# Performance work log

Hardware: AMD Instinct MI355X
Metric: run time of the kernel (lower is better)

Reference implementation:

```python
import jax, jax.numpy as jnp
import numpy as np


def _ffn(h, wu, wd):
    # SwiGLU: split w_up output into gate/up halves (torch chunk(2, dim=-1))
    gate, up = jnp.split(h @ wu, 2, axis=-1)
    return (jax.nn.silu(gate) * up) @ wd


def setup_inputs() -> dict:
    key = jax.random.key(0)
    ks = jax.random.split(key, 6)
    B, S, H, E, F = 4, 2048, 1024, 16, 512
    scale = 0.02
    x = jax.random.normal(ks[0], (B, S, H), dtype=jnp.float32)
    Wr = jax.random.normal(ks[1], (H, E), dtype=jnp.float32) * scale        # router (Linear, no bias)
    W_up = jax.random.normal(ks[2], (E, H, 2 * F), dtype=jnp.float32) * scale  # stacked expert w_up
    W_down = jax.random.normal(ks[3], (E, F, H), dtype=jnp.float32) * scale    # stacked expert w_down
    Ws_up = jax.random.normal(ks[4], (H, 2 * F), dtype=jnp.float32) * scale    # shared expert
    Ws_down = jax.random.normal(ks[5], (F, H), dtype=jnp.float32) * scale
    return {"x": x, "Wr": Wr, "W_up": W_up, "W_down": W_down,
            "Ws_up": Ws_up, "Ws_down": Ws_down, "num_active": 2}


def reference(x, Wr, W_up, W_down, Ws_up, Ws_down, num_active):
    B, S, H = x.shape
    E = Wr.shape[1]
    xf = x.reshape(-1, H)                     # [T, H]
    T = xf.shape[0]
    router_probs = jax.nn.softmax(xf @ Wr, axis=-1)            # [T, E]
    topk_p, topk_i = jax.lax.top_k(router_probs, num_active)   # [T, K]
    topk_p = topk_p / (topk_p.sum(-1, keepdims=True) + 1e-9)
    # dense per-token combine weights; 0 for non-selected experts, so the
    # dense per-expert compute below matches the masked gather/scatter math
    w = jnp.zeros((T, E), x.dtype).at[jnp.arange(T)[:, None], topk_i].set(topk_p)

    def step(acc, p):
        wu, wd, we = p                         # [H,2F], [F,H], [T]
        return acc + we[:, None] * _ffn(xf, wu, wd), None

    out, _ = jax.lax.scan(step, jnp.zeros_like(xf), (W_up, W_down, w.T))
    out = out + _ffn(xf, Ws_up, Ws_down)       # shared expert added to every token
    return out.reshape(B, S, H), router_probs
```

## Files before the change

kernel.cpp:

```cpp
#include <hip/hip_runtime.h>
#include <stdint.h>

#define T_TOK 8192
#define HD 1024
#define NE 16
#define NET 17
#define FD 512
#define CAP 8448
#define MAXWG 448
#define CPX 56

typedef unsigned int uint;
typedef unsigned short ushort;
typedef __attribute__((ext_vector_type(8))) __bf16 bf16x8;
typedef __attribute__((ext_vector_type(4))) float f32x4;

#define OFF_XBF   0ull
#define OFF_WUPT  16777216ull
#define OFF_WDT   52428800ull
#define OFF_ACT   70254592ull
#define OFF_EIDX  95420416ull
#define OFF_EW    95485952ull
#define OFF_TOK   95551488ull
#define OFF_WGT   96125952ull
#define OFF_META  96700416ull
#define OFF_SEL   96704512ull
#define WS_NEEDED (OFF_SEL + 131072ull)


__device__ __forceinline__ ushort f2bf(float f) {
    uint u = __float_as_uint(f);
    u += 0x7FFFu + ((u >> 16) & 1u);
    return (ushort)(u >> 16);
}
__device__ __forceinline__ float bf2f(ushort u) {
    return __uint_as_float(((uint)u) << 16);
}
__device__ __forceinline__ void gload16(const void* g, void* l) {
    __builtin_amdgcn_global_load_lds(
        (const __attribute__((address_space(1))) void*)g,
        (__attribute__((address_space(3))) void*)l, 16, 0, 0);
}

__global__ __launch_bounds__(1024) void k_router(const float* __restrict__ x,
                                                 const float* __restrict__ Wr,
                                                 float* __restrict__ probs,
                                                 ushort* __restrict__ xb,
                                                 int* __restrict__ tok,
                                                 float* __restrict__ wgt,
                                                 int4* __restrict__ sel) {
    __shared__ __align__(16) float wr_s[HD * NE];
    int tid = threadIdx.x;
    int t0 = blockIdx.x * 16;
#pragma unroll
    for (int i = 0; i < 4; ++i) {
        int idx = (i * 1024 + tid) * 4;
        *(float4*)(&wr_s[idx]) = *(const float4*)(Wr + idx);
    }
#pragma unroll
    for (int p = 0; p < 4; ++p) {
        int r = p * 4 + (tid >> 8);
        int c = (tid & 255) * 4;
        float4 v = *(const float4*)(x + (size_t)(t0 + r) * HD + c);
        ushort4 cc;
        cc.x = f2bf(v.x); cc.y = f2bf(v.y); cc.z = f2bf(v.z); cc.w = f2bf(v.w);
        *(ushort4*)(xb + (size_t)(t0 + r) * HD + c) = cc;
    }
    __syncthreads();
    int t = t0 + (tid >> 6);
    int sub = tid & 63;
    int e = sub & 15, kp = sub >> 4;
    const float* xg = x + (size_t)t * HD + kp * 256;
    const int wb = kp * 256 * NE + e;
    float s0 = 0.f, s1 = 0.f;
#pragma unroll 8
    for (int j = 0; j < 256; j += 4) {
        float4 v = *(const float4*)(xg + j);
        s0 = fmaf(v.x, wr_s[wb + (j + 0) * NE], s0);
        s1 = fmaf(v.y, wr_s[wb + (j + 1) * NE], s1);
        s0 = fmaf(v.z, wr_s[wb + (j + 2) * NE], s0);
        s1 = fmaf(v.w, wr_s[wb + (j + 3) * NE], s1);
    }
    float s = s0 + s1;
    s += __shfl_xor(s, 16);
    s += __shfl_xor(s, 32);
    float m = s;
#pragma unroll
    for (int w = 1; w < 16; w <<= 1) m = fmaxf(m, __shfl_xor(m, w));
    float p = __expf(s - m);
    float sum = p;
#pragma unroll
    for (int w = 1; w < 16; w <<= 1) sum += __shfl_xor(sum, w);
    p /= sum;
    if (kp == 0) probs[(size_t)t * NE + e] = p;
    float m1 = p;
#pragma unroll
    for (int w = 1; w < 16; w <<= 1) m1 = fmaxf(m1, __shfl_xor(m1, w));
    unsigned long long bal = __ballot(p == m1);
    int i1 = __ffs((int)((bal >> (kp * 16)) & 0xFFFFu)) - 1;
    float p2v = (e == i1) ? -1.f : p;
    float m2 = p2v;
#pragma unroll
    for (int w = 1; w < 16; w <<= 1) m2 = fmaxf(m2, __shfl_xor(m2, w));
    bal = __ballot(p2v == m2);
    int i2 = __ffs((int)((bal >> (kp * 16)) & 0xFFFFu)) - 1;
    if (sub == 0) {
        float inv2 = 1.f / (m1 + m2 + 1e-9f);
        sel[t] = make_int4(i1, i2, __float_as_int(m1 * inv2), __float_as_int(m2 * inv2));
        tok[16 * CAP + t] = t;
        wgt[16 * CAP + t] = 1.f;
    }
}

__global__ __launch_bounds__(1024) void k_bucket(const int4* __restrict__ sel,
                                                 int* __restrict__ tok,
                                                 float* __restrict__ wgt,
                                                 int2* __restrict__ inva,
                                                 int2* __restrict__ invb,
                                                 int* __restrict__ meta) {
    __shared__ int wcnt[16], wbase[16];
    int e = blockIdx.x;
    int wave = threadIdx.x >> 6;
    int lane = threadIdx.x & 63;
    unsigned long long ltmask = (1ull << lane) - 1ull;
    int tstart = wave * 512;
    int cnt = 0;
#pragma unroll
    for (int it = 0; it < 8; ++it) {
        int4 s = sel[tstart + it * 64 + lane];
        cnt += (int)__popcll(__ballot(s.x == e)) + (int)__popcll(__ballot(s.y == e));
    }
    if (lane == 0) wcnt[wave] = cnt;
    __syncthreads();
    if (threadIdx.x == 0) {
        int acc = 0;
#pragma unroll
        for (int w = 0; w < 16; ++w) { wbase[w] = acc; acc += wcnt[w]; }
        meta[e] = acc;
    }
    __syncthreads();
    int pos = wbase[wave];
#pragma unroll
    for (int it = 0; it < 8; ++it) {
        int t = tstart + it * 64 + lane;
        int4 s = sel[t];
        bool m1 = (s.x == e), m2 = (s.y == e);
        unsigned long long b1 = __ballot(m1), b2 = __ballot(m2);
        int c1 = (int)__popcll(b1);
        if (m1) {
            int q = pos + (int)__popcll(b1 & ltmask);
            tok[e * CAP + q] = t; wgt[e * CAP + q] = __int_as_float(s.z);
            inva[t] = make_int2(e, q);
        }
        if (m2) {
            int q = pos + c1 + (int)__popcll(b2 & ltmask);
            tok[e * CAP + q] = t; wgt[e * CAP + q] = __int_as_float(s.w);
            invb[t] = make_int2(e, q);
        }
        pos += c1 + (int)__popcll(b2);
    }
}

__global__ __launch_bounds__(256) void k_tup(const float* __restrict__ Wup,
                                             const float* __restrict__ Wsup,
                                             ushort* __restrict__ dst) {
    __shared__ __align__(16) float tile[64][68];
    int bid = blockIdx.x;
    int e = bid >> 8, rem = bid & 255;
    int h0 = (rem >> 4) * 64, n0 = (rem & 15) * 64;
    const float* src = (e < 16) ? (Wup + (size_t)e * HD * 1024) : Wsup;
    int tid = threadIdx.x;
    int rr = tid >> 4, cc = (tid & 15) * 4;
#pragma unroll
    for (int q = 0; q < 4; ++q) {
        float4 v = *(const float4*)(src + (size_t)(h0 + q * 16 + rr) * 1024 + n0 + cc);
        *(float4*)(&tile[q * 16 + rr][cc]) = v;
    }
    __syncthreads();
#pragma unroll
    for (int q = 0; q < 4; ++q) {
        int nl = q * 16 + rr;
        ushort4 o;
        o.x = f2bf(tile[cc + 0][nl]);
        o.y = f2bf(tile[cc + 1][nl]);
        o.z = f2bf(tile[cc + 2][nl]);
        o.w = f2bf(tile[cc + 3][nl]);
        *(ushort4*)(dst + (size_t)e * 1048576 + (size_t)(n0 + nl) * 1024 + h0 + cc) = o;
    }
}

__global__ __launch_bounds__(256) void k_tdn(const float* __restrict__ Wdn,
                                             const float* __restrict__ Wsdn,
                                             ushort* __restrict__ dst) {
    __shared__ __align__(16) float tile[64][68];
    int bid = blockIdx.x;
    int e = bid >> 7, rem = bid & 127;
    int f0 = (rem >> 4) * 64, h0 = (rem & 15) * 64;
    const float* src = (e < 16) ? (Wdn + (size_t)e * FD * HD) : Wsdn;
    int tid = threadIdx.x;
    int rr = tid >> 4, cc = (tid & 15) * 4;
#pragma unroll
    for (int q = 0; q < 4; ++q) {
        float4 v = *(const float4*)(src + (size_t)(f0 + q * 16 + rr) * 1024 + h0 + cc);
        *(float4*)(&tile[q * 16 + rr][cc]) = v;
    }
    __syncthreads();
#pragma unroll
    for (int q = 0; q < 4; ++q) {
        int hl = q * 16 + rr;
        ushort4 o;
        o.x = f2bf(tile[cc + 0][hl]);
        o.y = f2bf(tile[cc + 1][hl]);
        o.z = f2bf(tile[cc + 2][hl]);
        o.w = f2bf(tile[cc + 3][hl]);
        *(ushort4*)(dst + (size_t)e * 524288 + (size_t)(h0 + hl) * 512 + f0 + cc) = o;
    }
}

__global__ void k_finalize(int* __restrict__ meta, int* __restrict__ tok,
                           float* __restrict__ wgt) {
    __shared__ int sN[NET], sPad[NET];
    int tid = threadIdx.x;
    if (tid == 0) {
        meta[16] = T_TOK;
        int idx = 0, yoff = 0;
        for (int e = 0; e < NET; e++) {
            int n = meta[e];
            int padded = (n + 255) & ~255;
            sN[e] = n; sPad[e] = padded;
            meta[416 + e] = yoff;
            for (int i = 0; i < padded; i += 256) {
                meta[32 + idx] = e; meta[160 + idx] = i; meta[288 + idx] = yoff + i; idx++;
            }
            yoff += n;
        }
        meta[17] = idx;
    }
    __syncthreads();
    for (int e = 0; e < NET; e++)
        for (int i = sN[e] + tid; i < sPad[e]; i += 256) {
            tok[e * CAP + i] = 0; wgt[e * CAP + i] = 0.f;
        }
}

__global__ __launch_bounds__(512, 2) void k_up(const ushort* __restrict__ xb,
                                               const ushort* __restrict__ wupT,
                                               ushort* __restrict__ act,
                                               const int* __restrict__ tok,
                                               const int* __restrict__ meta) {
    __shared__ __align__(16) char smem[131072];
    int bid = blockIdx.x;
    int s = (bid & 7) * CPX + (bid >> 3);
    int rb = s >> 2, cb = s & 3;
    if (rb >= meta[17]) return;
    int e = meta[32 + rb], rloc = meta[160 + rb], abrow = meta[288 + rb];
    int ne = meta[e];
    int tid = threadIdx.x, lane = tid & 63, wave = tid >> 6;

    int srow = tid >> 3;
    int col16 = (tid & 7) << 4;
    int swz = col16 ^ ((srow & 7) << 4);
    const int listBase = e * CAP + rloc;
    int tokr[4];
#pragma unroll
    for (int i = 0; i < 4; i++) tokr[i] = tok[listBase + i * 64 + srow];
    const char* xbase = (const char*)xb;
    const char* wb = (const char*)wupT + (size_t)e * 2097152;
    int ldsl = wave * 1024;

    int wr = wave >> 1, wc = wave & 1;
    int lr = lane & 15, lk = lane >> 4;
    int aOff = (wr * 64 + lr) * 128;
    int bOff = (wc * 64 + lr) * 128;
    int kp0 = (lk * 16) ^ ((lr & 7) << 4);
    int kp1 = (64 + lk * 16) ^ ((lr & 7) << 4);

    f32x4 accg[4][4], accu[4][4];
#pragma unroll
    for (int m = 0; m < 4; m++)
#pragma unroll
        for (int n = 0; n < 4; n++) {
            accg[m][n] = (f32x4){0.f, 0.f, 0.f, 0.f};
            accu[m][n] = (f32x4){0.f, 0.f, 0.f, 0.f};
        }

#define STAGE_UP(KT, D)                                                                   \
    {                                                                                     \
        char* base = smem + (D) * 65536;                                                  \
        int kB = (KT) * 128;                                                              \
        _Pragma("unroll")                                                                 \
        for (int i = 0; i < 4; i++)                                                       \
            gload16(xbase + (size_t)tokr[i] * 2048 + kB + swz, base + i * 8192 + ldsl);   \
        _Pragma("unroll")                                                                 \
        for (int i = 0; i < 2; i++)                                                       \
            gload16(wb + (size_t)(cb * 128 + i * 64 + srow) * 2048 + kB + swz,            \
                    base + 32768 + i * 8192 + ldsl);                                      \
        _Pragma("unroll")                                                                 \
        for (int i = 0; i < 2; i++)                                                       \
            gload16(wb + (size_t)(512 + cb * 128 + i * 64 + srow) * 2048 + kB + swz,      \
                    base + 49152 + i * 8192 + ldsl);                                      \
    }

    STAGE_UP(0, 0);
    asm volatile("s_waitcnt vmcnt(0)" ::: "memory");
    __syncthreads();
    int cur = 0;
#pragma unroll 1
    for (int kt = 0; kt < 16; ++kt) {
        if (kt < 15) STAGE_UP(kt + 1, cur ^ 1);
        const char* A  = smem + cur * 65536;
        const char* Bg = A + 32768;
        const char* Bu = A + 49152;
#pragma unroll
        for (int kk = 0; kk < 2; kk++) {
            int kp = kk ? kp1 : kp0;
            bf16x8 a[4], bg[4], bu[4];
#pragma unroll
            for (int m = 0; m < 4; m++) a[m] = *(const bf16x8*)(A + aOff + m * 2048 + kp);
#pragma unroll
            for (int n = 0; n < 4; n++) bg[n] = *(const bf16x8*)(Bg + bOff + n * 2048 + kp);
#pragma unroll
            for (int n = 0; n < 4; n++) bu[n] = *(const bf16x8*)(Bu + bOff + n * 2048 + kp);
#pragma unroll
            for (int m = 0; m < 4; m++)
#pragma unroll
                for (int n = 0; n < 4; n++) {
                    accg[m][n] = __builtin_amdgcn_mfma_f32_16x16x32_bf16(a[m], bg[n], accg[m][n], 0, 0, 0);
                    accu[m][n] = __builtin_amdgcn_mfma_f32_16x16x32_bf16(a[m], bu[n], accu[m][n], 0, 0, 0);
                }
        }
        asm volatile("s_waitcnt vmcnt(0)" ::: "memory");
        __syncthreads();
        cur ^= 1;
    }
    ushort* actl = (ushort*)smem;
#pragma unroll
    for (int m = 0; m < 4; m++)
#pragma unroll
        for (int n = 0; n < 4; n++)
#pragma unroll
            for (int j = 0; j < 4; j++) {
                float gv = accg[m][n][j];
                float uv = accu[m][n][j];
                float av = (gv / (1.f + __expf(-gv))) * uv;
                int row = wr * 64 + m * 16 + lk * 4 + j;
                int col = wc * 64 + n * 16 + lr;
                actl[row * 128 + col] = f2bf(av);
            }
    __syncthreads();
#pragma unroll
    for (int p = 0; p < 8; p++) {
        int c = p * 512 + tid;
        int row = c >> 4, off = (c & 15) << 4;
        if (rloc + row < ne)
            *(uint4*)((char*)act + (size_t)(abrow + row) * 1024 + cb * 256 + off) =
                *(const uint4*)((const char*)actl + row * 256 + off);
    }
#undef STAGE_UP
}

__global__ __launch_bounds__(512, 2) void k_down(const ushort* __restrict__ act,
                                                 const ushort* __restrict__ wdT,
                                                 ushort* __restrict__ ybuf,
                                                 const float* __restrict__ wgt,
                                                 const int* __restrict__ meta) {
    __shared__ __align__(16) char smem[131072];
    int bid = blockIdx.x;
    int s = (bid & 7) * CPX + (bid >> 3);
    int rb = s >> 2, cb = s & 3;
    if (rb >= meta[17]) return;
    int e = meta[32 + rb], rloc = meta[160 + rb], abrow = meta[288 + rb];
    int ne = meta[e];
    int tid = threadIdx.x, lane = tid & 63, wave = tid >> 6;

    int srow = tid >> 3;
    int col16 = (tid & 7) << 4;
    int swz = col16 ^ ((srow & 7) << 4);
    const char* abase = (const char*)act + (size_t)abrow * 1024;
    const char* bbase = (const char*)wdT + (size_t)e * 1048576 + (size_t)cb * 256 * 1024;
    int ldsl = wave * 1024;

    int wr = wave >> 1, wc = wave & 1;
    int lr = lane & 15, lk = lane >> 4;
    int aOff = (wr * 64 + lr) * 128;
    int bOff = (wc * 128 + lr) * 128;
    int kp0 = (lk * 16) ^ ((lr & 7) << 4);
    int kp1 = (64 + lk * 16) ^ ((lr & 7) << 4);

    f32x4 acc[4][8];
#pragma unroll
    for (int m = 0; m < 4; m++)
#pragma unroll
        for (int n = 0; n < 8; n++) acc[m][n] = (f32x4){0.f, 0.f, 0.f, 0.f};

#define STAGE_DN(KT, D)                                                                  \
    {                                                                                    \
        char* base = smem + (D) * 65536;                                                 \
        int kB = (KT) * 128;                                                             \
        _Pragma("unroll")                                                                \
        for (int i = 0; i < 4; i++)                                                      \
            gload16(abase + (size_t)(i * 64 + srow) * 1024 + kB + swz,                   \
                    base + i * 8192 + ldsl);                                             \
        _Pragma("unroll")                                                                \
        for (int i = 0; i < 4; i++)                                                      \
            gload16(bbase + (size_t)(i * 64 + srow) * 1024 + kB + swz,                   \
                    base + 32768 + i * 8192 + ldsl);                                     \
    }

    STAGE_DN(0, 0);
    asm volatile("s_waitcnt vmcnt(0)" ::: "memory");
    __syncthreads();
    int cur = 0;
#pragma unroll 1
    for (int kt = 0; kt < 8; ++kt) {
        if (kt < 7) STAGE_DN(kt + 1, cur ^ 1);
        const char* A = smem + cur * 65536;
        const char* B = A + 32768;
#pragma unroll
        for (int kk = 0; kk < 2; kk++) {
            int kp = kk ? kp1 : kp0;
            bf16x8 a[4], b[8];
#pragma unroll
            for (int m = 0; m < 4; m++) a[m] = *(const bf16x8*)(A + aOff + m * 2048 + kp);
#pragma unroll
            for (int n = 0; n < 8; n++) b[n] = *(const bf16x8*)(B + bOff + n * 2048 + kp);
#pragma unroll
            for (int m = 0; m < 4; m++)
#pragma unroll
                for (int n = 0; n < 8; n++)
                    acc[m][n] = __builtin_amdgcn_mfma_f32_16x16x32_bf16(a[m], b[n], acc[m][n], 0, 0, 0);
        }
        asm volatile("s_waitcnt vmcnt(0)" ::: "memory");
        __syncthreads();
        cur ^= 1;
    }
    const int lb = e * CAP + rloc;
    ushort* yl = (ushort*)smem;
#pragma unroll
    for (int m = 0; m < 4; m++)
#pragma unroll
        for (int j = 0; j < 4; j++) {
            int row = wr * 64 + m * 16 + lk * 4 + j;
            float w = wgt[lb + row];
#pragma unroll
            for (int n = 0; n < 8; n++) {
                int col = wc * 128 + n * 16 + lr;
                yl[row * 256 + col] = f2bf(acc[m][n][j] * w);
            }
        }
    __syncthreads();
#pragma unroll
    for (int p = 0; p < 16; p++) {
        int c = p * 512 + tid;
        int row = c >> 5, off = (c & 31) << 4;
        if (rloc + row < ne)
            *(uint4*)((char*)ybuf + (size_t)(abrow + row) * 2048 + cb * 512 + off) =
                *(const uint4*)((const char*)yl + row * 512 + off);
    }
#undef STAGE_DN
}

__global__ __launch_bounds__(256) void k_combine(const ushort* __restrict__ y,
                                                 const int2* __restrict__ ia,
                                                 const int2* __restrict__ ib,
                                                 const int* __restrict__ meta,
                                                 float* __restrict__ out) {
    int t = blockIdx.x;
    int2 a = ia[t], b = ib[t];
    int r0 = (meta[416 + a.x] + a.y) << 10;
    int r1 = (meta[416 + b.x] + b.y) << 10;
    int rs = (meta[432] + t) << 10;
    int c = threadIdx.x << 2;
    ushort4 va = *(const ushort4*)(y + r0 + c);
    ushort4 vb = *(const ushort4*)(y + r1 + c);
    ushort4 vs = *(const ushort4*)(y + rs + c);
    float4 o;
    o.x = bf2f(va.x) + bf2f(vb.x) + bf2f(vs.x);
    o.y = bf2f(va.y) + bf2f(vb.y) + bf2f(vs.y);
    o.z = bf2f(va.z) + bf2f(vb.z) + bf2f(vs.z);
    o.w = bf2f(va.w) + bf2f(vb.w) + bf2f(vs.w);
    *(float4*)(out + ((size_t)t << 10) + c) = o;
}

extern "C" void kernel_launch(void* const* d_in, const int* in_sizes, int n_in,
                              void* d_out, int out_size, void* d_ws, size_t ws_size,
                              hipStream_t stream) {
    const float* x    = (const float*)d_in[0];
    const float* Wr   = (const float*)d_in[1];
    const float* Wup  = (const float*)d_in[2];
    const float* Wdn  = (const float*)d_in[3];
    const float* Wsup = (const float*)d_in[4];
    const float* Wsdn = (const float*)d_in[5];
    float* out = (float*)d_out;
    float* probs = out + (size_t)T_TOK * HD;

    if (ws_size < WS_NEEDED) return;

    char* ws = (char*)d_ws;
    ushort* xb    = (ushort*)(ws + OFF_XBF);
    ushort* wupT  = (ushort*)(ws + OFF_WUPT);
    ushort* wdT   = (ushort*)(ws + OFF_WDT);
    ushort* act   = (ushort*)(ws + OFF_ACT);
    int2*   inva  = (int2*)(ws + OFF_EIDX);
    int2*   invb  = (int2*)(ws + OFF_EW);
    int*    tok   = (int*)(ws + OFF_TOK);
    float*  wgt   = (float*)(ws + OFF_WGT);
    int*    meta  = (int*)(ws + OFF_META);
    int4*   sel   = (int4*)(ws + OFF_SEL);
    ushort* ybuf  = (ushort*)(ws + OFF_XBF);

    k_tup<<<NET * 256, 256, 0, stream>>>(Wup, Wsup, wupT);
    k_tdn<<<NET * 128, 256, 0, stream>>>(Wdn, Wsdn, wdT);
    k_router<<<T_TOK / 16, 1024, 0, stream>>>(x, Wr, probs, xb, tok, wgt, sel);
    k_bucket<<<NE, 1024, 0, stream>>>(sel, tok, wgt, inva, invb, meta);
    k_finalize<<<1, 256, 0, stream>>>(meta, tok, wgt);
    k_up<<<MAXWG, 512, 0, stream>>>(xb, wupT, act, tok, meta);
    k_down<<<MAXWG, 512, 0, stream>>>(act, wdT, ybuf, wgt, meta);
    k_combine<<<T_TOK, 256, 0, stream>>>(ybuf, inva, invb, meta, out);
}
```

Baseline: 184.9 us.

## Switch expert GEMMs to 4-stage 64-wide K pipeline with partial waitcnt

Both the up and down expert GEMM kernels move from a double-buffered 128-wide K tile, which waited on all loads every step, to a 4-slot ring of 64-wide K tiles. Loads run three stages ahead and use partial vmcnt waits, so global loads overlap MFMA work. The LDS layout drops the XOR swizzle for a plain 64-byte row stride, and MFMA sections are wrapped in s_setprio. The unswizzled layout may cause LDS bank conflicts on the fragment reads, and using only a raw s_barrier per step leaves less margin for reuse hazards in the ring.

```diff
diff --git a/kernel.cpp b/kernel.cpp
--- a/kernel.cpp
+++ b/kernel.cpp
@@ -257,23 +257,22 @@
     int ne = meta[e];
     int tid = threadIdx.x, lane = tid & 63, wave = tid >> 6;
 
-    int srow = tid >> 3;
-    int col16 = (tid & 7) << 4;
-    int swz = col16 ^ ((srow & 7) << 4);
+    int chunk = (tid & 3) << 4;
+    int tid16 = tid << 4;
     const int listBase = e * CAP + rloc;
-    int tokr[4];
-#pragma unroll
-    for (int i = 0; i < 4; i++) tokr[i] = tok[listBase + i * 64 + srow];
+    int r0 = tid >> 2;
+    int tokr0 = tok[listBase + r0];
+    int tokr1 = tok[listBase + 128 + r0];
     const char* xbase = (const char*)xb;
     const char* wb = (const char*)wupT + (size_t)e * 2097152;
-    int ldsl = wave * 1024;
+    const char* wbg = wb + (size_t)(cb * 128 + r0) * 2048;
+    const char* wbu = wb + (size_t)(512 + cb * 128 + r0) * 2048;
 
     int wr = wave >> 1, wc = wave & 1;
     int lr = lane & 15, lk = lane >> 4;
-    int aOff = (wr * 64 + lr) * 128;
-    int bOff = (wc * 64 + lr) * 128;
-    int kp0 = (lk * 16) ^ ((lr & 7) << 4);
-    int kp1 = (64 + lk * 16) ^ ((lr & 7) << 4);
+    int aoff  = (wr * 64 + lr) * 64 + lk * 16;
+    int bgoff = 16384 + (wc * 64 + lr) * 64 + lk * 16;
+    int buoff = 24576 + (wc * 64 + lr) * 64 + lk * 16;
 
     f32x4 accg[4][4], accu[4][4];
 #pragma unroll
@@ -284,55 +283,44 @@
             accu[m][n] = (f32x4){0.f, 0.f, 0.f, 0.f};
         }
 
-#define STAGE_UP(KT, D)                                                                   \
-    {                                                                                     \
-        char* base = smem + (D) * 65536;                                                  \
-        int kB = (KT) * 128;                                                              \
-        _Pragma("unroll")                                                                 \
-        for (int i = 0; i < 4; i++)                                                       \
-            gload16(xbase + (size_t)tokr[i] * 2048 + kB + swz, base + i * 8192 + ldsl);   \
-        _Pragma("unroll")                                                                 \
-        for (int i = 0; i < 2; i++)                                                       \
-            gload16(wb + (size_t)(cb * 128 + i * 64 + srow) * 2048 + kB + swz,            \
-                    base + 32768 + i * 8192 + ldsl);                                      \
-        _Pragma("unroll")                                                                 \
-        for (int i = 0; i < 2; i++)                                                       \
-            gload16(wb + (size_t)(512 + cb * 128 + i * 64 + srow) * 2048 + kB + swz,      \
-                    base + 49152 + i * 8192 + ldsl);                                      \
-    }
-
-    STAGE_UP(0, 0);
-    asm volatile("s_waitcnt vmcnt(0)" ::: "memory");
-    __syncthreads();
-    int cur = 0;
+#define STAGE_UP(KT)                                                          \
+    {                                                                         \
+        char* b_ = smem + ((KT) & 3) * 32768;                                 \
+        int kB_ = (KT) * 64;                                                  \
+        gload16(xbase + (size_t)tokr0 * 2048 + kB_ + chunk, b_ + tid16);      \
+        gload16(xbase + (size_t)tokr1 * 2048 + kB_ + chunk, b_ + 8192 + tid16); \
+        gload16(wbg + kB_ + chunk, b_ + 16384 + tid16);                       \
+        gload16(wbu + kB_ + chunk, b_ + 24576 + tid16);                       \
+    }
+
+    STAGE_UP(0); STAGE_UP(1); STAGE_UP(2);
 #pragma unroll 1
-    for (int kt = 0; kt < 16; ++kt) {
-        if (kt < 15) STAGE_UP(kt + 1, cur ^ 1);
-        const char* A  = smem + cur * 65536;
-        const char* Bg = A + 32768;
-        const char* Bu = A + 49152;
-#pragma unroll
-        for (int kk = 0; kk < 2; kk++) {
-            int kp = kk ? kp1 : kp0;
-            bf16x8 a[4], bg[4], bu[4];
-#pragma unroll
-            for (int m = 0; m < 4; m++) a[m] = *(const bf16x8*)(A + aOff + m * 2048 + kp);
-#pragma unroll
-            for (int n = 0; n < 4; n++) bg[n] = *(const bf16x8*)(Bg + bOff + n * 2048 + kp);
-#pragma unroll
-            for (int n = 0; n < 4; n++) bu[n] = *(const bf16x8*)(Bu + bOff + n * 2048 + kp);
-#pragma unroll
-            for (int m = 0; m < 4; m++)
-#pragma unroll
-                for (int n = 0; n < 4; n++) {
-                    accg[m][n] = __builtin_amdgcn_mfma_f32_16x16x32_bf16(a[m], bg[n], accg[m][n], 0, 0, 0);
-                    accu[m][n] = __builtin_amdgcn_mfma_f32_16x16x32_bf16(a[m], bu[n], accu[m][n], 0, 0, 0);
-                }
-        }
-        asm volatile("s_waitcnt vmcnt(0)" ::: "memory");
-        __syncthreads();
-        cur ^= 1;
-    }
+    for (int kt = 0; kt < 32; ++kt) {
+        if (kt < 30)      { asm volatile("s_waitcnt vmcnt(8)" ::: "memory"); }
+        else if (kt == 30){ asm volatile("s_waitcnt vmcnt(4)" ::: "memory"); }
+        else              { asm volatile("s_waitcnt vmcnt(0)" ::: "memory"); }
+        __builtin_amdgcn_s_barrier();
+        __builtin_amdgcn_sched_barrier(0);
+        if (kt < 29) STAGE_UP(kt + 3);
+        const char* B = smem + (kt & 3) * 32768;
+        bf16x8 a[4], bg[4], bu[4];
+#pragma unroll
+        for (int m = 0; m < 4; m++) a[m] = *(const bf16x8*)(B + aoff + m * 1024);
+#pragma unroll
+        for (int n = 0; n < 4; n++) bg[n] = *(const bf16x8*)(B + bgoff + n * 1024);
+#pragma unroll
+        for (int n = 0; n < 4; n++) bu[n] = *(const bf16x8*)(B + buoff + n * 1024);
+        __builtin_amdgcn_s_setprio(1);
+#pragma unroll
+        for (int m = 0; m < 4; m++)
+#pragma unroll
+            for (int n = 0; n < 4; n++) {
+                accg[m][n] = __builtin_amdgcn_mfma_f32_16x16x32_bf16(a[m], bg[n], accg[m][n], 0, 0, 0);
+                accu[m][n] = __builtin_amdgcn_mfma_f32_16x16x32_bf16(a[m], bu[n], accu[m][n], 0, 0, 0);
+            }
+        __builtin_amdgcn_s_setprio(0);
+    }
+    __syncthreads();
     ushort* actl = (ushort*)smem;
 #pragma unroll
     for (int m = 0; m < 4; m++)
@@ -373,19 +361,18 @@
     int ne = meta[e];
     int tid = threadIdx.x, lane = tid & 63, wave = tid >> 6;
 
-    int srow = tid >> 3;
-    int col16 = (tid & 7) << 4;
-    int swz = col16 ^ ((srow & 7) << 4);
-    const char* abase = (const char*)act + (size_t)abrow * 1024;
-    const char* bbase = (const char*)wdT + (size_t)e * 1048576 + (size_t)cb * 256 * 1024;
-    int ldsl = wave * 1024;
+    int chunk = (tid & 3) << 4;
+    int tid16 = tid << 4;
+    int r0 = tid >> 2;
+    const char* ab0 = (const char*)act + (size_t)(abrow + r0) * 1024;
+    const char* ab1 = ab0 + 128 * 1024;
+    const char* bb0 = (const char*)wdT + (size_t)e * 1048576 + (size_t)(cb * 256 + r0) * 1024;
+    const char* bb1 = bb0 + 128 * 1024;
 
     int wr = wave >> 1, wc = wave & 1;
     int lr = lane & 15, lk = lane >> 4;
-    int aOff = (wr * 64 + lr) * 128;
-    int bOff = (wc * 128 + lr) * 128;
-    int kp0 = (lk * 16) ^ ((lr & 7) << 4);
-    int kp1 = (64 + lk * 16) ^ ((lr & 7) << 4);
+    int aoff = (wr * 64 + lr) * 64 + lk * 16;
+    int boff = 16384 + (wc * 128 + lr) * 64 + lk * 16;
 
     f32x4 acc[4][8];
 #pragma unroll
@@ -393,47 +380,40 @@
 #pragma unroll
         for (int n = 0; n < 8; n++) acc[m][n] = (f32x4){0.f, 0.f, 0.f, 0.f};
 
-#define STAGE_DN(KT, D)                                                                  \
-    {                                                                                    \
-        char* base = smem + (D) * 65536;                                                 \
-        int kB = (KT) * 128;                                                             \
-        _Pragma("unroll")                                                                \
-        for (int i = 0; i < 4; i++)                                                      \
-            gload16(abase + (size_t)(i * 64 + srow) * 1024 + kB + swz,                   \
-                    base + i * 8192 + ldsl);                                             \
-        _Pragma("unroll")                                                                \
-        for (int i = 0; i < 4; i++)                                                      \
-            gload16(bbase + (size_t)(i * 64 + srow) * 1024 + kB + swz,                   \
-                    base + 32768 + i * 8192 + ldsl);                                     \
-    }
-
-    STAGE_DN(0, 0);
-    asm volatile("s_waitcnt vmcnt(0)" ::: "memory");
-    __syncthreads();
-    int cur = 0;
+#define STAGE_DN(KT)                                                          \
+    {                                                                         \
+        char* b_ = smem + ((KT) & 3) * 32768;                                 \
+        int kB_ = (KT) * 64;                                                  \
+        gload16(ab0 + kB_ + chunk, b_ + tid16);                               \
+        gload16(ab1 + kB_ + chunk, b_ + 8192 + tid16);                        \
+        gload16(bb0 + kB_ + chunk, b_ + 16384 + tid16);                       \
+        gload16(bb1 + kB_ + chunk, b_ + 24576 + tid16);                       \
+    }
+
+    STAGE_DN(0); STAGE_DN(1); STAGE_DN(2);
 #pragma unroll 1
-    for (int kt = 0; kt < 8; ++kt) {
-        if (kt < 7) STAGE_DN(kt + 1, cur ^ 1);
-        const char* A = smem + cur * 65536;
-        const char* B = A + 32768;
-#pragma unroll
-        for (int kk = 0; kk < 2; kk++) {
-            int kp = kk ? kp1 : kp0;
-            bf16x8 a[4], b[8];
-#pragma unroll
-            for (int m = 0; m < 4; m++) a[m] = *(const bf16x8*)(A + aOff + m * 2048 + kp);
-#pragma unroll
-            for (int n = 0; n < 8; n++) b[n] = *(const bf16x8*)(B + bOff + n * 2048 + kp);
-#pragma unroll
-            for (int m = 0; m < 4; m++)
-#pragma unroll
-                for (int n = 0; n < 8; n++)
-                    acc[m][n] = __builtin_amdgcn_mfma_f32_16x16x32_bf16(a[m], b[n], acc[m][n], 0, 0, 0);
-        }
-        asm volatile("s_waitcnt vmcnt(0)" ::: "memory");
-        __syncthreads();
-        cur ^= 1;
-    }
+    for (int kt = 0; kt < 16; ++kt) {
+        if (kt < 14)      { asm volatile("s_waitcnt vmcnt(8)" ::: "memory"); }
+        else if (kt == 14){ asm volatile("s_waitcnt vmcnt(4)" ::: "memory"); }
+        else              { asm volatile("s_waitcnt vmcnt(0)" ::: "memory"); }
+        __builtin_amdgcn_s_barrier();
+        __builtin_amdgcn_sched_barrier(0);
+        if (kt < 13) STAGE_DN(kt + 3);
+        const char* B = smem + (kt & 3) * 32768;
+        bf16x8 a[4], b[8];
+#pragma unroll
+        for (int m = 0; m < 4; m++) a[m] = *(const bf16x8*)(B + aoff + m * 1024);
+#pragma unroll
+        for (int n = 0; n < 8; n++) b[n] = *(const bf16x8*)(B + boff + n * 1024);
+        __builtin_amdgcn_s_setprio(1);
+#pragma unroll
+        for (int m = 0; m < 4; m++)
+#pragma unroll
+            for (int n = 0; n < 8; n++)
+                acc[m][n] = __builtin_amdgcn_mfma_f32_16x16x32_bf16(a[m], b[n], acc[m][n], 0, 0, 0);
+        __builtin_amdgcn_s_setprio(0);
+    }
+    __syncthreads();
     const int lb = e * CAP + rloc;
     ushort* yl = (ushort*)smem;
 #pragma unroll
```

Result: slower. 203.9 us (+10.3%).
